# Kernel optimization log

Measured on AMD Instinct MI355X. Metric: run time of the kernel, lower is better.

The kernel has to match this reference:

```python
import jax, jax.numpy as jnp
import numpy as np

NEG = -1e30  # safe log-zero for fp32/bf16


def _ctc_neg_log_likelihood(labels, log_probs, label_length, data_length, blank):
    """Standard CTC alpha (forward) DP in log space.
    labels: [B, L] int, log_probs: [T, B, C], lengths: [B] int.
    Returns per-example negative log likelihood [B]."""
    T, B, C = log_probs.shape
    L = labels.shape[1]
    S = 2 * L + 1  # extended label: blank, l1, blank, l2, ..., blank
    ext = jnp.full((B, S), blank, dtype=labels.dtype).at[:, 1::2].set(labels)
    prev2 = jnp.concatenate([jnp.full((B, 2), -1, labels.dtype), ext[:, :-2]], axis=1)
    allow_skip = (ext != blank) & (ext != prev2)  # [B, S] skip-transition legality

    def emit(lp_t):  # [B, C] -> [B, S]
        return jnp.take_along_axis(lp_t, ext, axis=1)

    # t = 0: paths can only be at s=0 (blank) or s=1 (first label)
    alpha0 = jnp.where(jnp.arange(S)[None, :] < 2, emit(log_probs[0]), NEG)

    def step(alpha, xs):
        lp_t, t = xs
        a1 = jnp.concatenate([jnp.full((B, 1), NEG, alpha.dtype), alpha[:, :-1]], axis=1)
        a2 = jnp.concatenate([jnp.full((B, 2), NEG, alpha.dtype), alpha[:, :-2]], axis=1)
        a2 = jnp.where(allow_skip, a2, NEG)
        new = jax.nn.logsumexp(jnp.stack([alpha, a1, a2]), axis=0) + emit(lp_t)
        # freeze alpha once past this example's sequence length
        return jnp.where((t < data_length)[:, None], new, alpha), None

    alpha, _ = jax.lax.scan(step, alpha0, (log_probs[1:], jnp.arange(1, T)))

    # likelihood = alpha[2*len] (final blank) + alpha[2*len - 1] (final label)
    a_blank = jnp.take_along_axis(alpha, (2 * label_length)[:, None], axis=1)[:, 0]
    a_label = jnp.take_along_axis(alpha, (2 * label_length - 1)[:, None], axis=1)[:, 0]
    return -jnp.logaddexp(a_blank, a_label)


def setup_inputs() -> dict:
    key = jax.random.key(0)
    k1, k2, k3, k4 = jax.random.split(key, 4)
    T, B, C, L = 1024, 32, 1024, 128
    data = jax.random.normal(k1, (T, B, C), dtype=jnp.float32)
    labels = jax.random.randint(k2, (B, L), 1, C, dtype=jnp.int32)  # avoid blank=0
    label_length = jax.random.randint(k3, (B,), 64, L + 1, dtype=jnp.int32)
    data_length = jax.random.randint(k4, (B,), 512, T + 1, dtype=jnp.int32)
    return {"labels": labels, "data": data, "label_length": label_length,
            "data_length": data_length}


def reference(labels, data, label_length, data_length):
    # from_logits=True -> ctc_loss_v2: log_softmax then CTC; blank_index=0
    log_probs = jax.nn.log_softmax(data, axis=-1)
    loss = _ctc_neg_log_likelihood(labels, log_probs, label_length, data_length, 0)
    return jnp.mean(loss).reshape([1])
```

## Files before the change

### kernel.cpp

```cpp
#include <hip/hip_runtime.h>
#include <hip/hip_bf16.h>

#define T_DIM 1024
#define B_DIM 32
#define C_DIM 1024
#define L_DIM 128
#define S_DIM 257
#define TPAD  (T_DIM + 64)

__global__ __launch_bounds__(256) void emit_kernel(const float* __restrict__ data,
                                                   const int* __restrict__ labels,
                                                   float2* __restrict__ epair,
                                                   float* __restrict__ eblank) {
    const int wave = threadIdx.x >> 6;
    const int lane = threadIdx.x & 63;
    const int row = blockIdx.x * 4 + wave;
    const int b = row & (B_DIM - 1);
    const int t = row >> 5;

    const float4* d4 = (const float4*)(data + (size_t)row * C_DIM);
    float4 v[4];
    float m = -3.4e38f;
#pragma unroll
    for (int k = 0; k < 4; ++k) {
        v[k] = d4[lane + 64 * k];
        m = fmaxf(m, fmaxf(fmaxf(v[k].x, v[k].y), fmaxf(v[k].z, v[k].w)));
    }
#pragma unroll
    for (int off = 32; off >= 1; off >>= 1)
        m = fmaxf(m, __shfl_xor(m, off, 64));
    float s = 0.f;
#pragma unroll
    for (int k = 0; k < 4; ++k)
        s += __expf(v[k].x - m) + __expf(v[k].y - m) +
             __expf(v[k].z - m) + __expf(v[k].w - m);
#pragma unroll
    for (int off = 32; off >= 1; off >>= 1)
        s += __shfl_xor(s, off, 64);
    const float lse = m + __logf(s);

    const float* drow = data + (size_t)row * C_DIM;
    const int2 cc = ((const int2*)(labels + b * L_DIM))[lane];
    float2 pr;
    pr.x = __expf(drow[cc.x] - lse);
    pr.y = __expf(drow[cc.y] - lse);
    epair[(size_t)row * 64 + lane] = pr;
    if (lane == 0) eblank[b * TPAD + t] = __expf(drow[0] - lse);
}

__global__ __launch_bounds__(64, 1) void dp_kernel(const float2* __restrict__ epair,
                                                   const float* __restrict__ eblank,
                                                   const int* __restrict__ labels,
                                                   const int* __restrict__ label_length,
                                                   const int* __restrict__ data_length,
                                                   float* __restrict__ lossbuf) {
    const int b = blockIdx.x;
    const int l = threadIdx.x;
    const int* lab = labels + b * L_DIM;
    const int len = label_length[b];
    const int dlen = data_length[b];

    const int2 cc = ((const int2*)lab)[l];
    const int cprev = (l > 0) ? lab[2 * l - 1] : -1;
    const double skip1d = ((l > 0) && (cc.x != cprev)) ? 1.0 : 0.0;
    const double skip3d = (cc.y != cc.x) ? 1.0 : 0.0;

    const float* ebrow = eblank + b * TPAD;

    double a0, a1, a2 = 0.0, a3 = 0.0, a4 = 0.0;
    {
        const float2 e0 = epair[(size_t)b * 64 + l];
        const float eb0 = ebrow[0];
        a0 = (l == 0) ? (double)eb0 : 0.0;
        a1 = (l == 0) ? (double)e0.x : 0.0;
    }
    long long kacc = 0;

    auto step = [&](float2 epv, float ebv) {
        const double e1 = (double)epv.x, e2 = (double)epv.y, eb = (double)ebv;
        double h = __shfl_up(a3, 1, 64);
        if (l == 0) h = 0.0;
        const double n0 = (a0 + h) * eb;
        const double n1 = fma(skip1d, h, a1 + a0) * e1;
        const double n2 = (a2 + a1) * eb;
        const double n3 = fma(skip3d, a1, a3 + a2) * e2;
        const double n4 = (a4 + a3) * eb;
        a0 = n0; a1 = n1; a2 = n2; a3 = n3; a4 = n4;
    };

    auto renorm = [&]() {
        double m = fmax(fmax(fmax(a0, a1), fmax(a2, a3)), a4);
#pragma unroll
        for (int off = 32; off >= 1; off >>= 1)
            m = fmax(m, __shfl_xor(m, off, 64));
        const long long mb = __double_as_longlong(m);
        const int ex = (int)((mb >> 52) & 0x7ff) - 1023;
        const double sc = __longlong_as_double((long long)(1023 - ex) << 52);
        a0 *= sc; a1 *= sc; a2 *= sc; a3 *= sc; a4 *= sc;
        kacc += ex;
    };

    float2 bufA[16], bufB[16];
    float ebA[16], ebB[16];

    auto load_chunk = [&](int c, float2* ep, float* eb) {
        const int t0 = 1 + 16 * c;
#pragma unroll
        for (int j = 0; j < 16; ++j) {
            ep[j] = epair[(size_t)((t0 + j) * B_DIM + b) * 64 + l];
            eb[j] = ebrow[t0 + j];
        }
    };

    auto compute_chunk = [&](int c, const float2* ep, const float* eb) {
        const int t0 = 1 + 16 * c;
        if (t0 + 15 < dlen) {
#pragma unroll
            for (int j = 0; j < 16; ++j) step(ep[j], eb[j]);
        } else {
#pragma unroll
            for (int j = 0; j < 16; ++j)
                if (t0 + j < dlen) step(ep[j], eb[j]);
        }
    };

    const int nch = (dlen - 1 + 15) / 16;
    load_chunk(0, bufA, ebA);
    load_chunk(1, bufB, ebB);
    __builtin_amdgcn_sched_barrier(0);
    for (int c = 0; c < nch; c += 2) {
        compute_chunk(c, bufA, ebA);
        load_chunk(c + 2, bufA, ebA);
        __builtin_amdgcn_sched_barrier(0);
        compute_chunk(c + 1, bufB, ebB);
        load_chunk(c + 3, bufB, ebB);
        __builtin_amdgcn_sched_barrier(0);
        renorm();
    }

    __shared__ double fin[S_DIM];
    fin[4 * l + 0] = a0; fin[4 * l + 1] = a1;
    fin[4 * l + 2] = a2; fin[4 * l + 3] = a3;
    if (l == 63) fin[256] = a4;
    __syncthreads();
    if (l == 0) {
        const double v = fin[2 * len] + fin[2 * len - 1];
        const long long vb = __double_as_longlong(v);
        const int ve = (int)((vb >> 52) & 0x7ff) - 1023;
        const double mant = __longlong_as_double(
            (vb & 0x000FFFFFFFFFFFFFLL) | (1023LL << 52));
        const double l2 = (double)__log2f((float)mant) + (double)ve + (double)kacc;
        lossbuf[b] = (float)(-l2 * 0.6931471805599453);
    }
}

__global__ __launch_bounds__(64) void final_kernel(const float* __restrict__ lossbuf,
                                                   float* __restrict__ out) {
    const int l = threadIdx.x;
    float v = (l < B_DIM) ? lossbuf[l] : 0.f;
#pragma unroll
    for (int off = 32; off >= 1; off >>= 1)
        v += __shfl_xor(v, off, 64);
    if (l == 0) out[0] = v * (1.0f / B_DIM);
}

extern "C" void kernel_launch(void* const* d_in, const int* in_sizes, int n_in,
                              void* d_out, int out_size, void* d_ws, size_t ws_size,
                              hipStream_t stream) {
    const int*   labels       = (const int*)d_in[0];
    const float* data         = (const float*)d_in[1];
    const int*   label_length = (const int*)d_in[2];
    const int*   data_length  = (const int*)d_in[3];
    float*       out          = (float*)d_out;

    float2* epair  = (float2*)d_ws;
    float*  eblank = (float*)((char*)d_ws + (size_t)TPAD * B_DIM * 64 * sizeof(float2));
    float*  lossb  = eblank + (size_t)B_DIM * TPAD;

    const int rows = T_DIM * B_DIM;
    emit_kernel<<<rows / 4, 256, 0, stream>>>(data, labels, epair, eblank);
    dp_kernel<<<B_DIM, 64, 0, stream>>>(epair, eblank, labels, label_length,
                                        data_length, lossb);
    final_kernel<<<1, 64, 0, stream>>>(lossb, out);
}
```

Baseline: 271.3 us.

## Split CTC DP into forward alpha and backward beta halves meeting midpoint

Runs the sequential CTC recursion from both ends at once: one block per example computes alpha up to the midpoint of the data length while another computes beta backward from the end. A new combine kernel joins the two vectors with the transition structure to recover the likelihood. This roughly halves the serial dependency chain, which bounds the latency of the DP kernel. The emission layout moves to batch-major, per-chunk rows are staged into LDS via global_load_lds with double buffering, and the renorm reduces only the high word. In exchange it adds an extra kernel launch and a more complex midpoint join that must handle boundaries and skip rules correctly.

Result: faster. 254.1 us (-6.3%).

```diff
diff --git a/kernel.cpp b/kernel.cpp
--- a/kernel.cpp
+++ b/kernel.cpp
@@ -6,7 +6,14 @@
 #define C_DIM 1024
 #define L_DIM 128
 #define S_DIM 257
-#define TPAD  (T_DIM + 64)
+#define CH    32
+
+#define WS_EPAIR   0
+#define WS_EBLANK  (32u * 1024u * 64u * 8u)
+#define WS_ALPHA   (WS_EBLANK + 32u * 1024u * 4u)
+#define WS_BETA    (WS_ALPHA + 32u * 264u * 8u)
+#define WS_KACC    (WS_BETA + 32u * 264u * 8u)
+#define WS_LOSS    (WS_KACC + 32u * 2u * 8u)
 
 __global__ __launch_bounds__(256) void emit_kernel(const float* __restrict__ data,
                                                    const int* __restrict__ labels,
@@ -44,8 +51,8 @@
     float2 pr;
     pr.x = __expf(drow[cc.x] - lse);
     pr.y = __expf(drow[cc.y] - lse);
-    epair[(size_t)row * 64 + lane] = pr;
-    if (lane == 0) eblank[b * TPAD + t] = __expf(drow[0] - lse);
+    epair[((size_t)b * T_DIM + t) * 64 + lane] = pr;
+    if (lane == 0) eblank[b * T_DIM + t] = __expf(drow[0] - lse);
 }
 
 __global__ __launch_bounds__(64, 1) void dp_kernel(const float2* __restrict__ epair,
@@ -53,103 +60,196 @@
                                                    const int* __restrict__ labels,
                                                    const int* __restrict__ label_length,
                                                    const int* __restrict__ data_length,
-                                                   float* __restrict__ lossbuf) {
-    const int b = blockIdx.x;
+                                                   double* __restrict__ alphavec,
+                                                   double* __restrict__ betavec,
+                                                   long long* __restrict__ kaccs) {
+    const int b   = blockIdx.x & (B_DIM - 1);
+    const int dir = blockIdx.x >> 5;
     const int l = threadIdx.x;
     const int* lab = labels + b * L_DIM;
     const int len = label_length[b];
     const int dlen = data_length[b];
-
-    const int2 cc = ((const int2*)lab)[l];
-    const int cprev = (l > 0) ? lab[2 * l - 1] : -1;
-    const double skip1d = ((l > 0) && (cc.x != cprev)) ? 1.0 : 0.0;
-    const double skip3d = (cc.y != cc.x) ? 1.0 : 0.0;
-
-    const float* ebrow = eblank + b * TPAD;
-
-    double a0, a1, a2 = 0.0, a3 = 0.0, a4 = 0.0;
-    {
-        const float2 e0 = epair[(size_t)b * 64 + l];
-        const float eb0 = ebrow[0];
-        a0 = (l == 0) ? (double)eb0 : 0.0;
-        a1 = (l == 0) ? (double)e0.x : 0.0;
-    }
+    const int m = dlen >> 1;
+
+    __shared__ float2 ebuf[2][CH][64];
+    __shared__ float  ebl[T_DIM];
+
+    const float2* eprow = epair + (size_t)b * T_DIM * 64;
+    const float*  ebrow = eblank + (size_t)b * T_DIM;
+
+#pragma unroll
+    for (int i = 0; i < T_DIM / 64; ++i)
+        __builtin_amdgcn_global_load_lds(
+            (const __attribute__((address_space(1))) void*)(ebrow + i * 64 + l),
+            (__attribute__((address_space(3))) void*)(&ebl[i * 64]), 4, 0, 0);
+
+    auto stage_chunk = [&](int cb, int trow0) {
+#pragma unroll
+        for (int i = 0; i < CH / 2; ++i)
+            __builtin_amdgcn_global_load_lds(
+                (const __attribute__((address_space(1))) void*)
+                    ((const char*)(eprow + (size_t)(trow0 + 2 * i) * 64) + l * 16),
+                (__attribute__((address_space(3))) void*)(&ebuf[cb][2 * i][0]), 16, 0, 0);
+    };
+
+    double a0 = 0.0, a1 = 0.0, a2 = 0.0, a3 = 0.0, a4 = 0.0;
     long long kacc = 0;
 
-    auto step = [&](float2 epv, float ebv) {
-        const double e1 = (double)epv.x, e2 = (double)epv.y, eb = (double)ebv;
-        double h = __shfl_up(a3, 1, 64);
-        if (l == 0) h = 0.0;
-        const double n0 = (a0 + h) * eb;
-        const double n1 = fma(skip1d, h, a1 + a0) * e1;
-        const double n2 = (a2 + a1) * eb;
-        const double n3 = fma(skip3d, a1, a3 + a2) * e2;
-        const double n4 = (a4 + a3) * eb;
-        a0 = n0; a1 = n1; a2 = n2; a3 = n3; a4 = n4;
-    };
-
     auto renorm = [&]() {
-        double m = fmax(fmax(fmax(a0, a1), fmax(a2, a3)), a4);
+        double mx = fmax(fmax(fmax(a0, a1), fmax(a2, a3)), a4);
+        int hi = __double2hiint(mx);
 #pragma unroll
         for (int off = 32; off >= 1; off >>= 1)
-            m = fmax(m, __shfl_xor(m, off, 64));
-        const long long mb = __double_as_longlong(m);
-        const int ex = (int)((mb >> 52) & 0x7ff) - 1023;
-        const double sc = __longlong_as_double((long long)(1023 - ex) << 52);
+            hi = max(hi, __shfl_xor(hi, off, 64));
+        const int ex = ((hi >> 20) & 0x7ff) - 1023;
+        const double sc = __hiloint2double((1023 - ex) << 20, 0);
         a0 *= sc; a1 *= sc; a2 *= sc; a3 *= sc; a4 *= sc;
         kacc += ex;
     };
 
-    float2 bufA[16], bufB[16];
-    float ebA[16], ebB[16];
-
-    auto load_chunk = [&](int c, float2* ep, float* eb) {
-        const int t0 = 1 + 16 * c;
-#pragma unroll
-        for (int j = 0; j < 16; ++j) {
-            ep[j] = epair[(size_t)((t0 + j) * B_DIM + b) * 64 + l];
-            eb[j] = ebrow[t0 + j];
-        }
-    };
-
-    auto compute_chunk = [&](int c, const float2* ep, const float* eb) {
-        const int t0 = 1 + 16 * c;
-        if (t0 + 15 < dlen) {
-#pragma unroll
-            for (int j = 0; j < 16; ++j) step(ep[j], eb[j]);
-        } else {
-#pragma unroll
-            for (int j = 0; j < 16; ++j)
-                if (t0 + j < dlen) step(ep[j], eb[j]);
-        }
-    };
-
-    const int nch = (dlen - 1 + 15) / 16;
-    load_chunk(0, bufA, ebA);
-    load_chunk(1, bufB, ebB);
-    __builtin_amdgcn_sched_barrier(0);
-    for (int c = 0; c < nch; c += 2) {
-        compute_chunk(c, bufA, ebA);
-        load_chunk(c + 2, bufA, ebA);
-        __builtin_amdgcn_sched_barrier(0);
-        compute_chunk(c + 1, bufB, ebB);
-        load_chunk(c + 3, bufB, ebB);
-        __builtin_amdgcn_sched_barrier(0);
-        renorm();
+    if (dir == 0) {
+        const int2 cc = ((const int2*)lab)[l];
+        const double skip1d = ((l > 0) && (cc.x != lab[2 * l - 1])) ? 1.0 : 0.0;
+        const double skip3d = (cc.y != cc.x) ? 1.0 : 0.0;
+
+        stage_chunk(0, 1);
+        __builtin_amdgcn_s_waitcnt(0x0f70);
+
+        {
+            const float2 ep0 = eprow[l];
+            a0 = (l == 0) ? (double)ebl[0] : 0.0;
+            a1 = (l == 0) ? (double)ep0.x : 0.0;
+        }
+
+        const int nsteps = m - 1;
+        const int nch = (nsteps + CH - 1) / CH;
+        for (int c = 0; c < nch; ++c) {
+            const int cb = c & 1;
+            const bool more = (c + 1 < nch);
+            if (more) stage_chunk(cb ^ 1, 1 + CH * (c + 1));
+            __builtin_amdgcn_sched_barrier(0);
+            const int t0 = 1 + CH * c;
+            const bool full = (t0 + CH <= m);
+#pragma unroll
+            for (int j = 0; j < CH; ++j) {
+                if (full || (t0 + j < m)) {
+                    const float2 ep = ebuf[cb][j][l];
+                    const double eb = (double)ebl[t0 + j];
+                    double h = __shfl_up(a3, 1, 64);
+                    if (l == 0) h = 0.0;
+                    const double n0 = (a0 + h) * eb;
+                    const double n1 = fma(skip1d, h, a1 + a0) * (double)ep.x;
+                    const double n2 = (a2 + a1) * eb;
+                    const double n3 = fma(skip3d, a1, a3 + a2) * (double)ep.y;
+                    const double n4 = (a4 + a3) * eb;
+                    a0 = n0; a1 = n1; a2 = n2; a3 = n3; a4 = n4;
+                }
+            }
+            renorm();
+            if (more) __builtin_amdgcn_s_waitcnt(0x0f70);
+            __builtin_amdgcn_sched_barrier(0);
+        }
+
+        double* av = (double*)alphavec + b * 264;
+        av[4 * l + 0] = a0; av[4 * l + 1] = a1;
+        av[4 * l + 2] = a2; av[4 * l + 3] = a3;
+        if (l == 63) av[256] = a4;
+        if (l == 0) kaccs[2 * b + 0] = kacc;
+    } else {
+        const int2 c2 = ((const int2*)lab)[63 - l];
+        const int labL = (l > 0) ? lab[128 - 2 * l] : -1;
+        const double skip1d = ((l > 0) && (labL != c2.y)) ? 1.0 : 0.0;
+        const double skip3d = (c2.y != c2.x) ? 1.0 : 0.0;
+
+        stage_chunk(0, dlen - 1 - CH);
+        __builtin_amdgcn_s_waitcnt(0x0f70);
+
+        {
+            const float2 epi = eprow[(size_t)(dlen - 1) * 64 + (63 - l)];
+            const double ebi = (double)ebl[dlen - 1];
+            const int s0 = 256 - 4 * l;
+            a0 = (s0 == 2 * len     || s0 == 2 * len - 1) ? ebi : 0.0;
+            a1 = (s0 - 1 == 2 * len || s0 - 1 == 2 * len - 1) ? (double)epi.y : 0.0;
+            a2 = (s0 - 2 == 2 * len || s0 - 2 == 2 * len - 1) ? ebi : 0.0;
+            a3 = (s0 - 3 == 2 * len || s0 - 3 == 2 * len - 1) ? (double)epi.x : 0.0;
+            a4 = 0.0;
+        }
+
+        const int nsteps = dlen - 1 - m;
+        const int nch = (nsteps + CH - 1) / CH;
+        for (int c = 0; c < nch; ++c) {
+            const int cb = c & 1;
+            const bool more = (c + 1 < nch);
+            const int thi = dlen - 2 - CH * c;
+            const int tlo = thi - CH + 1;
+            if (more) stage_chunk(cb ^ 1, tlo - CH);
+            __builtin_amdgcn_sched_barrier(0);
+            const bool full = (tlo >= m);
+#pragma unroll
+            for (int jj = 0; jj < CH; ++jj) {
+                const int j = CH - 1 - jj;
+                const int t = tlo + j;
+                if (full || (t >= m)) {
+                    const float2 ep = ebuf[cb][j][63 - l];
+                    const double eb = (double)ebl[t];
+                    double h = __shfl_up(a3, 1, 64);
+                    if (l == 0) h = 0.0;
+                    const double n0 = (a0 + h) * eb;
+                    const double n1 = fma(skip1d, h, a1 + a0) * (double)ep.y;
+                    const double n2 = (a2 + a1) * eb;
+                    const double n3 = fma(skip3d, a1, a3 + a2) * (double)ep.x;
+                    const double n4 = (a4 + a3) * eb;
+                    a0 = n0; a1 = n1; a2 = n2; a3 = n3; a4 = n4;
+                }
+            }
+            renorm();
+            if (more) __builtin_amdgcn_s_waitcnt(0x0f70);
+            __builtin_amdgcn_sched_barrier(0);
+        }
+
+        double* bv = (double*)betavec + b * 264;
+        bv[256 - 4 * l] = a0; bv[255 - 4 * l] = a1;
+        bv[254 - 4 * l] = a2; bv[253 - 4 * l] = a3;
+        if (l == 63) bv[0] = a4;
+        if (l == 0) { bv[257] = 0.0; bv[258] = 0.0; kaccs[2 * b + 1] = kacc; }
     }
-
-    __shared__ double fin[S_DIM];
-    fin[4 * l + 0] = a0; fin[4 * l + 1] = a1;
-    fin[4 * l + 2] = a2; fin[4 * l + 3] = a3;
-    if (l == 63) fin[256] = a4;
-    __syncthreads();
+}
+
+__global__ __launch_bounds__(64) void combine_kernel(const double* __restrict__ alphavec,
+                                                     const double* __restrict__ betavec,
+                                                     const long long* __restrict__ kaccs,
+                                                     const int* __restrict__ labels,
+                                                     float* __restrict__ lossbuf) {
+    const int b = blockIdx.x;
+    const int l = threadIdx.x;
+    const double* A = alphavec + b * 264;
+    const double* Bv = betavec + b * 264;
+    const int* lab = labels + b * L_DIM;
+
+    const double a0 = A[4 * l], a1 = A[4 * l + 1], a2 = A[4 * l + 2], a3 = A[4 * l + 3];
+    const double b0 = Bv[4 * l], b1 = Bv[4 * l + 1], b2 = Bv[4 * l + 2];
+    const double b3 = Bv[4 * l + 3], b4 = Bv[4 * l + 4], b5 = Bv[4 * l + 5];
+    const double sk1 = (lab[2 * l + 1] != lab[2 * l]) ? 1.0 : 0.0;
+    const int labn = (l < 63) ? lab[2 * l + 2] : -1;
+    const double sk3 = ((l < 63) && (labn != lab[2 * l + 1])) ? 1.0 : 0.0;
+
+    double s = a0 * (b0 + b1)
+             + a1 * (b1 + b2 + sk1 * b3)
+             + a2 * (b2 + b3)
+             + a3 * (b3 + b4 + sk3 * b5);
+    if (l == 63) s += A[256] * Bv[256];
+
+#pragma unroll
+    for (int off = 32; off >= 1; off >>= 1)
+        s += __shfl_xor(s, off, 64);
+
     if (l == 0) {
-        const double v = fin[2 * len] + fin[2 * len - 1];
-        const long long vb = __double_as_longlong(v);
+        const long long k = kaccs[2 * b] + kaccs[2 * b + 1];
+        const long long vb = __double_as_longlong(s);
         const int ve = (int)((vb >> 52) & 0x7ff) - 1023;
         const double mant = __longlong_as_double(
             (vb & 0x000FFFFFFFFFFFFFLL) | (1023LL << 52));
-        const double l2 = (double)__log2f((float)mant) + (double)ve + (double)kacc;
+        const double l2 = (double)__log2f((float)mant) + (double)ve + (double)k;
         lossbuf[b] = (float)(-l2 * 0.6931471805599453);
     }
 }
@@ -173,13 +273,18 @@
     const int*   data_length  = (const int*)d_in[3];
     float*       out          = (float*)d_out;
 
-    float2* epair  = (float2*)d_ws;
-    float*  eblank = (float*)((char*)d_ws + (size_t)TPAD * B_DIM * 64 * sizeof(float2));
-    float*  lossb  = eblank + (size_t)B_DIM * TPAD;
+    char* ws = (char*)d_ws;
+    float2*    epair    = (float2*)(ws + WS_EPAIR);
+    float*     eblank   = (float*)(ws + WS_EBLANK);
+    double*    alphavec = (double*)(ws + WS_ALPHA);
+    double*    betavec  = (double*)(ws + WS_BETA);
+    long long* kaccs    = (long long*)(ws + WS_KACC);
+    float*     lossb    = (float*)(ws + WS_LOSS);
 
     const int rows = T_DIM * B_DIM;
     emit_kernel<<<rows / 4, 256, 0, stream>>>(data, labels, epair, eblank);
-    dp_kernel<<<B_DIM, 64, 0, stream>>>(epair, eblank, labels, label_length,
-                                        data_length, lossb);
+    dp_kernel<<<2 * B_DIM, 64, 0, stream>>>(epair, eblank, labels, label_length,
+                                            data_length, alphavec, betavec, kaccs);
+    combine_kernel<<<B_DIM, 64, 0, stream>>>(alphavec, betavec, kaccs, labels, lossb);
     final_kernel<<<1, 64, 0, stream>>>(lossb, out);
 }
```
